# Optimization experiments

Measured on AMD Instinct MI355X. Metric: run time of the kernel, lower is better.

## Reference

```python
import jax, jax.numpy as jnp
import numpy as np

MUL = 128      # multiplicity of 0e and 1o irreps
K = 4          # number of node-attr scalar channels (elements)
DIM = MUL + MUL * 3  # 512 flattened irrep dim


def setup_inputs() -> dict:
    key = jax.random.key(0)
    k1, k2, k3, k4, k5, k6, k7 = jax.random.split(key, 7)
    N = 100000
    m_i = jax.random.normal(k1, (N, DIM), dtype=jnp.float32)
    node_feats = jax.random.normal(k2, (N, DIM), dtype=jnp.float32)
    node_attrs = jax.random.uniform(k3, (N, K), dtype=jnp.float32)
    # o3.Linear internal weights: one [mul_in, mul_out] block per irrep (0e, 1o)
    W_lin0 = jax.random.normal(k4, (MUL, MUL), dtype=jnp.float32)
    W_lin1 = jax.random.normal(k5, (MUL, MUL), dtype=jnp.float32)
    # FullyConnectedTensorProduct weights: one [u, v, w] tensor per path
    # paths: (0e x 0e -> 0e) and (1o x 0e -> 1o); CG for l x 0 -> l is identity
    W_tp0 = jax.random.normal(k6, (MUL, K, MUL), dtype=jnp.float32)
    W_tp1 = jax.random.normal(k7, (MUL, K, MUL), dtype=jnp.float32)
    return {"m_i": m_i, "node_feats": node_feats, "node_attrs": node_attrs,
            "W_lin0": W_lin0, "W_lin1": W_lin1, "W_tp0": W_tp0, "W_tp1": W_tp1}


def _split(x):
    # [N, 512] -> ([N, 128] scalars, [N, 128, 3] vectors)
    s = x[:, :MUL]
    v = x[:, MUL:].reshape(x.shape[0], MUL, 3)
    return s, v


def reference(m_i, node_feats, node_attrs, W_lin0, W_lin1, W_tp0, W_tp1):
    N = m_i.shape[0]
    inv_lin = 1.0 / np.sqrt(MUL)          # e3nn Linear path normalization (fan_in = mul_in)
    inv_tp = 1.0 / np.sqrt(MUL * K)       # FCTP path normalization (fan_in = mul1*mul2)

    m0, m1 = _split(m_i)
    f0, f1 = _split(node_feats)

    # o3.Linear on hidden irreps: block-diagonal per-irrep matmul over multiplicity
    lin0 = (m0 @ W_lin0) * inv_lin                               # [N, 128]
    lin1 = jnp.einsum('num,uw->nwm', m1, W_lin1) * inv_lin       # [N, 128, 3]

    # FullyConnectedTensorProduct(feats, attrs): attrs are 0e scalars so CG is trivial
    tp0 = jnp.einsum('nu,nv,uvw->nw', f0, node_attrs, W_tp0) * inv_tp        # [N, 128]
    tp1 = jnp.einsum('num,nv,uvw->nwm', f1, node_attrs, W_tp1) * inv_tp      # [N, 128, 3]

    out0 = lin0 + tp0
    out1 = (lin1 + tp1).reshape(N, MUL * 3)
    return jnp.concatenate([out0, out1], axis=1)  # [N, 512]
```

## Files before the change

kernel.cpp:

```cpp
#include <hip/hip_runtime.h>


#define MUL 128
#define DIM 512
#define KTOT 640
#define NSTEPS 20
#define NODES 16
#define INV_LIN 0.08838834764831845f
#define INV_TP  0.04419417382415922f

typedef float f32x4 __attribute__((ext_vector_type(4)));
typedef __bf16 bf16x8 __attribute__((ext_vector_type(8)));

__device__ inline unsigned short f2bf(float x) {
    unsigned u = __float_as_uint(x);
    u += 0x7fffu + ((u >> 16) & 1u);
    return (unsigned short)(u >> 16);
}

__global__ __launch_bounds__(256) void prep_weights(
        const float* __restrict__ Wl0, const float* __restrict__ Wl1,
        const float* __restrict__ Wt0, const float* __restrict__ Wt1,
        unsigned short* __restrict__ P0, unsigned short* __restrict__ P1) {
    int idx = blockIdx.x * 256 + threadIdx.x;
    if (idx >= 2 * MUL * KTOT) return;
    int mat = idx / (MUL * KTOT);
    int r   = idx % (MUL * KTOT);
    int w = r / KTOT, k = r % KTOT;
    const float* Wl = mat ? Wl1 : Wl0;
    const float* Wt = mat ? Wt1 : Wt0;
    int sec = k >> 7, u = k & 127;
    float val;
    if (sec == 0) {
        val = Wl[u * MUL + w] * INV_LIN;
    } else {
        val = Wt[u * 512 + (sec - 1) * 128 + w] * INV_TP;
    }
    int ct = w >> 5, ct2 = (w >> 4) & 1, lr = w & 15;
    int ks = k >> 5, g = (k >> 3) & 3, i = k & 7;
    (mat ? P1 : P0)[((((ct * NSTEPS + ks) * 2 + ct2) * 64 + g * 16 + lr) << 3) + i] = f2bf(val);
}

#define POOL_BYTES 34816
__global__ __launch_bounds__(256, 8) void k_fused(
        const float* __restrict__ m_i, const float* __restrict__ nf,
        const float* __restrict__ attrs,
        const bf16x8* __restrict__ P0, const bf16x8* __restrict__ P1,
        float* __restrict__ out, int N) {
    __shared__ __align__(16) char pool[POOL_BYTES];
    __bf16 (*Mde)[NODES][136] = (__bf16(*)[NODES][136])(pool);
    __bf16 (*Fde)[NODES][136] = (__bf16(*)[NODES][136])(pool + 17408);

    int tid = threadIdx.x;
    int ct = tid >> 6, l = tid & 63;
    int lr = l & 15, g = l >> 4;

    long nodeBase = (long)blockIdx.x * NODES;

    for (int c = tid; c < NODES * 128; c += 256) {
        int nl = c >> 7, q = c & 127;
        long node = nodeBase + nl; if (node >= N) node = N - 1;
        f32x4 x = *(const f32x4*)&m_i[node * DIM + q * 4];
        f32x4 y = *(const f32x4*)&nf [node * DIM + q * 4];
        #pragma unroll
        for (int j = 0; j < 4; ++j) {
            int col = q * 4 + j;
            int cls, u;
            if (col < 128) { cls = 0; u = col; }
            else { int cc = col - 128; cls = 1 + cc % 3; u = cc / 3; }
            Mde[cls][nl][u] = (__bf16)x[j];
            Fde[cls][nl][u] = (__bf16)y[j];
        }
    }

    f32x4 acc[4][2] = {};
    __syncthreads();

    #pragma unroll
    for (int ks = 0; ks < 4; ++ks) {
        bf16x8 b0[2], b1[2];
        #pragma unroll
        for (int c2 = 0; c2 < 2; ++c2) {
            b0[c2] = P0[((ct * NSTEPS + ks) * 2 + c2) * 64 + l];
            b1[c2] = P1[((ct * NSTEPS + ks) * 2 + c2) * 64 + l];
        }
        #pragma unroll
        for (int cls = 0; cls < 4; ++cls) {
            bf16x8 af = *(const bf16x8*)&Mde[cls][lr][ks * 32 + g * 8];
            #pragma unroll
            for (int c2 = 0; c2 < 2; ++c2)
                acc[cls][c2] = __builtin_amdgcn_mfma_f32_16x16x32_bf16(
                    af, cls ? b1[c2] : b0[c2], acc[cls][c2], 0, 0, 0);
        }
    }

    #pragma unroll 1
    for (int v = 0; v < 4; ++v) {
        float atv[4];
        #pragma unroll
        for (int r = 0; r < 4; ++r) {
            long nd = nodeBase + g * 4 + r; if (nd >= N) nd = N - 1;
            atv[r] = attrs[nd * 4 + v];
        }
        #pragma unroll
        for (int cls = 0; cls < 4; ++cls) {
            const bf16x8* Pm = cls ? P1 : P0;
            f32x4 t2[2] = {};
            #pragma unroll
            for (int ks = 0; ks < 4; ++ks) {
                int kst = (1 + v) * 4 + ks;
                bf16x8 b[2];
                b[0] = Pm[((ct * NSTEPS + kst) * 2 + 0) * 64 + l];
                b[1] = Pm[((ct * NSTEPS + kst) * 2 + 1) * 64 + l];
                bf16x8 af = *(const bf16x8*)&Fde[cls][lr][ks * 32 + g * 8];
                #pragma unroll
                for (int c2 = 0; c2 < 2; ++c2)
                    t2[c2] = __builtin_amdgcn_mfma_f32_16x16x32_bf16(
                        af, b[c2], t2[c2], 0, 0, 0);
            }
            #pragma unroll
            for (int c2 = 0; c2 < 2; ++c2)
                #pragma unroll
                for (int r = 0; r < 4; ++r)
                    acc[cls][c2][r] += atv[r] * t2[c2][r];
        }
    }

    __syncthreads();
    float (*Ost)[DIM] = (float(*)[DIM])pool;
    #pragma unroll
    for (int c2 = 0; c2 < 2; ++c2) {
        int wv_ = ct * 32 + c2 * 16 + lr;
        #pragma unroll
        for (int r = 0; r < 4; ++r) {
            int nl = g * 4 + r;
            Ost[nl][wv_]               = acc[0][c2][r];
            Ost[nl][128 + wv_ * 3 + 0] = acc[1][c2][r];
            Ost[nl][128 + wv_ * 3 + 1] = acc[2][c2][r];
            Ost[nl][128 + wv_ * 3 + 2] = acc[3][c2][r];
        }
    }
    __syncthreads();
    for (int c = tid; c < NODES * 128; c += 256) {
        int nl = c >> 7, q = c & 127;
        long node = nodeBase + nl;
        if (node < N)
            *(f32x4*)&out[node * DIM + q * 4] = *(const f32x4*)&Ost[nl][q * 4];
    }
}

extern "C" void kernel_launch(void* const* d_in, const int* in_sizes, int n_in,
                              void* d_out, int out_size, void* d_ws, size_t ws_size,
                              hipStream_t stream) {
    const float* m_i  = (const float*)d_in[0];
    const float* nf   = (const float*)d_in[1];
    const float* attr = (const float*)d_in[2];
    const float* Wl0  = (const float*)d_in[3];
    const float* Wl1  = (const float*)d_in[4];
    const float* Wt0  = (const float*)d_in[5];
    const float* Wt1  = (const float*)d_in[6];
    float* out = (float*)d_out;
    int N = in_sizes[0] / DIM;

    unsigned short* P0 = (unsigned short*)d_ws;
    unsigned short* P1 = P0 + MUL * KTOT;

    int prep_total = 2 * MUL * KTOT;
    hipLaunchKernelGGL(prep_weights, dim3((prep_total + 255) / 256), dim3(256), 0, stream,
                       Wl0, Wl1, Wt0, Wt1, P0, P1);
    hipLaunchKernelGGL(k_fused, dim3((N + NODES - 1) / NODES), dim3(256), 0, stream,
                       m_i, nf, attr, (const bf16x8*)P0, (const bf16x8*)P1, out, N);
}
```

Baseline: 243.6 us.

## Pre-scale features by attrs in LDS and double node tile per block

The block now handles 32 nodes with 512 threads, each wave covering 16 nodes and 32 output columns. The tensor-product path no longer runs a separate MFMA reduction per attr channel followed by a scalar FMA. Instead each attr-scaled copy of the features is written into a shared LDS buffer, and all five K-phases accumulate directly into one accumulator. This removes the per-phase scalar epilogue and lowers weight-load traffic per node. In exchange it adds extra LDS rewrites and barriers between phases, rounds the attr-scaled features to bf16, and doubles LDS per block, which lowers occupancy.

```diff
diff --git a/kernel.cpp b/kernel.cpp
--- a/kernel.cpp
+++ b/kernel.cpp
@@ -5,7 +5,7 @@
 #define DIM 512
 #define KTOT 640
 #define NSTEPS 20
-#define NODES 16
+#define NODES 32
 #define INV_LIN 0.08838834764831845f
 #define INV_TP  0.04419417382415922f
 
@@ -41,23 +41,24 @@
     (mat ? P1 : P0)[((((ct * NSTEPS + ks) * 2 + ct2) * 64 + g * 16 + lr) << 3) + i] = f2bf(val);
 }
 
-#define POOL_BYTES 34816
-__global__ __launch_bounds__(256, 8) void k_fused(
+#define POOL_BYTES 69632
+__global__ __launch_bounds__(512, 4) void k_fused(
         const float* __restrict__ m_i, const float* __restrict__ nf,
         const float* __restrict__ attrs,
         const bf16x8* __restrict__ P0, const bf16x8* __restrict__ P1,
         float* __restrict__ out, int N) {
     __shared__ __align__(16) char pool[POOL_BYTES];
-    __bf16 (*Mde)[NODES][136] = (__bf16(*)[NODES][136])(pool);
-    __bf16 (*Fde)[NODES][136] = (__bf16(*)[NODES][136])(pool + 17408);
+    __bf16 (*Abuf)[NODES][136] = (__bf16(*)[NODES][136])(pool);
+    __bf16 (*Fde)[NODES][136]  = (__bf16(*)[NODES][136])(pool + 34816);
 
     int tid = threadIdx.x;
-    int ct = tid >> 6, l = tid & 63;
+    int wv = tid >> 6, l = tid & 63;
     int lr = l & 15, g = l >> 4;
+    int ct = wv >> 1, nt = wv & 1;
 
     long nodeBase = (long)blockIdx.x * NODES;
 
-    for (int c = tid; c < NODES * 128; c += 256) {
+    for (int c = tid; c < NODES * 128; c += 512) {
         int nl = c >> 7, q = c & 127;
         long node = nodeBase + nl; if (node >= N) node = N - 1;
         f32x4 x = *(const f32x4*)&m_i[node * DIM + q * 4];
@@ -68,61 +69,49 @@
             int cls, u;
             if (col < 128) { cls = 0; u = col; }
             else { int cc = col - 128; cls = 1 + cc % 3; u = cc / 3; }
-            Mde[cls][nl][u] = (__bf16)x[j];
-            Fde[cls][nl][u] = (__bf16)y[j];
+            Abuf[cls][nl][u] = (__bf16)x[j];
+            Fde[cls][nl][u]  = (__bf16)y[j];
         }
     }
 
     f32x4 acc[4][2] = {};
     __syncthreads();
 
-    #pragma unroll
-    for (int ks = 0; ks < 4; ++ks) {
-        bf16x8 b0[2], b1[2];
-        #pragma unroll
-        for (int c2 = 0; c2 < 2; ++c2) {
-            b0[c2] = P0[((ct * NSTEPS + ks) * 2 + c2) * 64 + l];
-            b1[c2] = P1[((ct * NSTEPS + ks) * 2 + c2) * 64 + l];
+    #pragma unroll 1
+    for (int p = 0; p < 5; ++p) {
+        if (p > 0) {
+            __syncthreads();
+            int v = p - 1;
+            for (int c = tid; c < 4 * NODES * 16; c += 512) {
+                int qc = c & 15, nl = (c >> 4) & 31, cls = c >> 9;
+                long node = nodeBase + nl; if (node >= N) node = N - 1;
+                float at = attrs[node * 4 + v];
+                bf16x8 f = *(const bf16x8*)&Fde[cls][nl][qc * 8];
+                bf16x8 a;
+                #pragma unroll
+                for (int j = 0; j < 8; ++j)
+                    a[j] = (__bf16)((float)f[j] * at);
+                *(bf16x8*)&Abuf[cls][nl][qc * 8] = a;
+            }
+            __syncthreads();
         }
-        #pragma unroll
-        for (int cls = 0; cls < 4; ++cls) {
-            bf16x8 af = *(const bf16x8*)&Mde[cls][lr][ks * 32 + g * 8];
+        #pragma unroll 1
+        for (int kk = 0; kk < 4; ++kk) {
+            int kst = p * 4 + kk;
+            bf16x8 b0[2], b1[2];
             #pragma unroll
-            for (int c2 = 0; c2 < 2; ++c2)
-                acc[cls][c2] = __builtin_amdgcn_mfma_f32_16x16x32_bf16(
-                    af, cls ? b1[c2] : b0[c2], acc[cls][c2], 0, 0, 0);
-        }
-    }
-
-    #pragma unroll 1
-    for (int v = 0; v < 4; ++v) {
-        float atv[4];
-        #pragma unroll
-        for (int r = 0; r < 4; ++r) {
-            long nd = nodeBase + g * 4 + r; if (nd >= N) nd = N - 1;
-            atv[r] = attrs[nd * 4 + v];
-        }
-        #pragma unroll
-        for (int cls = 0; cls < 4; ++cls) {
-            const bf16x8* Pm = cls ? P1 : P0;
-            f32x4 t2[2] = {};
+            for (int c2 = 0; c2 < 2; ++c2) {
+                b0[c2] = P0[((ct * NSTEPS + kst) * 2 + c2) * 64 + l];
+                b1[c2] = P1[((ct * NSTEPS + kst) * 2 + c2) * 64 + l];
+            }
             #pragma unroll
-            for (int ks = 0; ks < 4; ++ks) {
-                int kst = (1 + v) * 4 + ks;
-                bf16x8 b[2];
-                b[0] = Pm[((ct * NSTEPS + kst) * 2 + 0) * 64 + l];
-                b[1] = Pm[((ct * NSTEPS + kst) * 2 + 1) * 64 + l];
-                bf16x8 af = *(const bf16x8*)&Fde[cls][lr][ks * 32 + g * 8];
+            for (int cls = 0; cls < 4; ++cls) {
+                bf16x8 af = *(const bf16x8*)&Abuf[cls][nt * 16 + lr][kk * 32 + g * 8];
                 #pragma unroll
                 for (int c2 = 0; c2 < 2; ++c2)
-                    t2[c2] = __builtin_amdgcn_mfma_f32_16x16x32_bf16(
-                        af, b[c2], t2[c2], 0, 0, 0);
+                    acc[cls][c2] = __builtin_amdgcn_mfma_f32_16x16x32_bf16(
+                        af, cls ? b1[c2] : b0[c2], acc[cls][c2], 0, 0, 0);
             }
-            #pragma unroll
-            for (int c2 = 0; c2 < 2; ++c2)
-                #pragma unroll
-                for (int r = 0; r < 4; ++r)
-                    acc[cls][c2][r] += atv[r] * t2[c2][r];
         }
     }
 
@@ -133,7 +122,7 @@
         int wv_ = ct * 32 + c2 * 16 + lr;
         #pragma unroll
         for (int r = 0; r < 4; ++r) {
-            int nl = g * 4 + r;
+            int nl = nt * 16 + g * 4 + r;
             Ost[nl][wv_]               = acc[0][c2][r];
             Ost[nl][128 + wv_ * 3 + 0] = acc[1][c2][r];
             Ost[nl][128 + wv_ * 3 + 1] = acc[2][c2][r];
@@ -141,7 +130,7 @@
         }
     }
     __syncthreads();
-    for (int c = tid; c < NODES * 128; c += 256) {
+    for (int c = tid; c < NODES * 128; c += 512) {
         int nl = c >> 7, q = c & 127;
         long node = nodeBase + nl;
         if (node < N)
@@ -168,6 +157,6 @@
     int prep_total = 2 * MUL * KTOT;
     hipLaunchKernelGGL(prep_weights, dim3((prep_total + 255) / 256), dim3(256), 0, stream,
                        Wl0, Wl1, Wt0, Wt1, P0, P1);
-    hipLaunchKernelGGL(k_fused, dim3((N + NODES - 1) / NODES), dim3(256), 0, stream,
+    hipLaunchKernelGGL(k_fused, dim3((N + NODES - 1) / NODES), dim3(512), 0, stream,
                        m_i, nf, attr, (const bf16x8*)P0, (const bf16x8*)P1, out, N);
 }
```

Result: no change. 242.8 us (-0.3%).
